# Performance work log

Measured on AMD Instinct MI355X. Metric: run time of the kernel, lower is better.

The kernel has to match this reference:

```python
import jax, jax.numpy as jnp
import numpy as np


def gcn_conv(x, src, dst, W, b, n_nodes):
    """PyG-style GCNConv: add self-loops, symmetric deg^-1/2 normalization,
    linear transform, scatter-add aggregation to dst, then bias."""
    loop = jnp.arange(n_nodes, dtype=src.dtype)
    s = jnp.concatenate([src, loop])
    d = jnp.concatenate([dst, loop])
    deg = jax.ops.segment_sum(jnp.ones_like(d, x.dtype), d, num_segments=n_nodes)
    dinv = jax.lax.rsqrt(deg)  # deg >= 1 due to self-loops
    norm = dinv[s] * dinv[d]  # [E+N]
    h = x @ W.T  # [N, out]
    msg = h[s] * norm[:, None]  # [E+N, out]
    return jax.ops.segment_sum(msg, d, num_segments=n_nodes) + b


def setup_inputs() -> dict:
    key = jax.random.key(0)
    k = jax.random.split(key, 6)
    N, E, IN, HID, OUT = 100000, 1600000, 128, 128, 64
    x = jax.random.normal(k[0], (N, IN), dtype=jnp.float32)
    edge_index = jax.random.randint(k[1], (2, E), 0, N, dtype=jnp.int64)
    W1 = jax.random.normal(k[2], (HID, IN), dtype=jnp.float32) * 0.05
    b1 = jnp.zeros((HID,), dtype=jnp.float32)
    W2 = jax.random.normal(k[3], (OUT, HID), dtype=jnp.float32) * 0.05
    b2 = jnp.zeros((OUT,), dtype=jnp.float32)
    return {"x": x, "W1": W1, "b1": b1, "W2": W2, "b2": b2, "edge_index": edge_index}


def reference(x, W1, b1, W2, b2, edge_index):
    n_nodes = x.shape[0]
    src, dst = edge_index[0], edge_index[1]
    h = jax.nn.relu(gcn_conv(x, src, dst, W1, b1, n_nodes))
    return gcn_conv(h, src, dst, W2, b2, n_nodes)
```

## Files before the change

### kernel.cpp

```cpp
#include <hip/hip_runtime.h>
#include <hip/hip_bf16.h>


#define IN_F  128
#define HID_F 128
#define OUT_F 64

#define NPB     128
#define MAXBKT  1024
#define CHUNK   2048
#define CAP     4096
#define SLAB    4096

typedef __bf16 bf16_t;
typedef __bf16 bf16x4 __attribute__((ext_vector_type(4)));
typedef __bf16 bf16x8 __attribute__((ext_vector_type(8)));
typedef float  f32x4  __attribute__((ext_vector_type(4)));

__global__ __launch_bounds__(256) void k_hist(const int* __restrict__ dst, int E,
                                              int* __restrict__ chunkhist, int NBKT,
                                              int pchunks,
                                              const float* __restrict__ W1s,
                                              const float* __restrict__ W2s,
                                              bf16_t* __restrict__ Wdst,
                                              int n1, int n2,
                                              int* __restrict__ bcur) {
    if ((int)blockIdx.x >= pchunks) {
        int i = (blockIdx.x - pchunks) * 256 + threadIdx.x;
        if (i < n1) Wdst[i] = (bf16_t)W1s[i];
        else if (i < n1 + n2) Wdst[i] = (bf16_t)W2s[i - n1];
        else if (i < n1 + n2 + NBKT) bcur[i - n1 - n2] = (i - n1 - n2) * SLAB;
        return;
    }
    __shared__ int cnt[MAXBKT];
    for (int i = threadIdx.x; i < NBKT; i += 256) cnt[i] = 0;
    __syncthreads();
    int base = blockIdx.x * CHUNK;
    for (int i = threadIdx.x; i < CHUNK; i += 256) {
        int e = base + i;
        if (e < E) atomicAdd(&cnt[dst[e] >> 7], 1);
    }
    __syncthreads();
    int* ch = chunkhist + (size_t)blockIdx.x * MAXBKT;
    for (int i = threadIdx.x; i < NBKT; i += 256) ch[i] = cnt[i];
}

__global__ __launch_bounds__(256) void k_part(const int* __restrict__ src,
                                              const int* __restrict__ dst, int E,
                                              int* __restrict__ bcur,
                                              const int* __restrict__ chunkhist,
                                              unsigned* __restrict__ part, int NBKT) {
    __shared__ int cnt[MAXBKT];
    __shared__ int base[MAXBKT];
    const int* ch = chunkhist + (size_t)blockIdx.x * MAXBKT;
    for (int i = threadIdx.x; i < NBKT; i += 256) {
        int c = ch[i];
        base[i] = c ? atomicAdd(&bcur[i], c) : 0;
        cnt[i] = 0;
    }
    __syncthreads();
    int cbase = blockIdx.x * CHUNK;
    for (int i = threadIdx.x; i < CHUNK; i += 256) {
        int e = cbase + i;
        if (e < E) {
            int d = dst[e];
            int b = d >> 7;
            int lp = atomicAdd(&cnt[b], 1);
            part[base[b] + lp] = (unsigned)src[e] | ((unsigned)(d & 127) << 17);
        }
    }
}

__global__ __launch_bounds__(256) void k_bucket(const unsigned* __restrict__ part,
                                                const int* __restrict__ bcur,
                                                int2* __restrict__ off2,
                                                int* __restrict__ col,
                                                float* __restrict__ dinv, int N) {
    __shared__ int lcnt[NPB];
    __shared__ int lexc[NPB];
    __shared__ int lcur[NPB];
    __shared__ int stage[CAP];
    int b = blockIdx.x;
    int t = threadIdx.x;
    int node0 = b * NPB;
    int nb = min(NPB, N - node0);
    int e0s = b * SLAB;
    int cnt = bcur[b] - e0s;
    if (t < NPB) lcnt[t] = 0;
    __syncthreads();
    for (int i = t; i < cnt; i += 256)
        atomicAdd(&lcnt[part[e0s + i] >> 17], 1);
    __syncthreads();
    if (t < NPB) lexc[t] = lcnt[t];
    __syncthreads();
    for (int ofs = 1; ofs < NPB; ofs <<= 1) {
        int add = (t >= ofs && t < NPB) ? lexc[t - ofs] : 0;
        __syncthreads();
        if (t < NPB) lexc[t] += add;
        __syncthreads();
    }
    if (t < NPB) {
        int ex = lexc[t] - lcnt[t];
        lcur[t] = ex;
        if (t < nb) {
            off2[node0 + t] = make_int2(e0s + ex, e0s + ex + lcnt[t]);
            dinv[node0 + t] = rsqrtf((float)lcnt[t] + 1.0f);
        }
    }
    __syncthreads();
    for (int i = t; i < cnt; i += 256) {
        unsigned p = part[e0s + i];
        int dl = p >> 17;
        int sv = (int)(p & 0x1FFFF);
        int lp = atomicAdd(&lcur[dl], 1);
        if (lp < CAP) stage[lp] = sv;
        else col[e0s + lp] = sv;
    }
    __syncthreads();
    for (int i = t; i < cnt && i < CAP; i += 256) col[e0s + i] = stage[i];
}

template <int NCOL, typename TIN>
__global__ __launch_bounds__(256) void k_gemm_mfma(const TIN* __restrict__ X,
                                                   const bf16_t* __restrict__ W,
                                                   const float* __restrict__ scale,
                                                   bf16_t* __restrict__ H, int N) {
    constexpr int CT = NCOL / 16;
    int wv = threadIdx.x >> 6, lane = threadIdx.x & 63;
    int quad = lane >> 4, l16 = lane & 15;
    int row0 = blockIdx.x * 128 + wv * 32;
    f32x4 acc[2][CT] = {};
#pragma unroll
    for (int ks = 0; ks < 4; ks++) {
        int k0 = ks * 32 + quad * 8;
        bf16x8 a[2];
#pragma unroll
        for (int rt = 0; rt < 2; rt++) {
            int r = row0 + rt * 16 + l16;
            if (r >= N) r = N - 1;
            const TIN* p = X + (size_t)r * 128 + k0;
            if constexpr (sizeof(TIN) == 4) {
                f32x4 x0 = *(const f32x4*)p;
                f32x4 x1 = *(const f32x4*)(p + 4);
                bf16x8 tt;
                tt[0] = (bf16_t)x0[0]; tt[1] = (bf16_t)x0[1];
                tt[2] = (bf16_t)x0[2]; tt[3] = (bf16_t)x0[3];
                tt[4] = (bf16_t)x1[0]; tt[5] = (bf16_t)x1[1];
                tt[6] = (bf16_t)x1[2]; tt[7] = (bf16_t)x1[3];
                a[rt] = tt;
            } else {
                a[rt] = *(const bf16x8*)p;
            }
        }
#pragma unroll
        for (int ct = 0; ct < CT; ct++) {
            bf16x8 bfrag = *(const bf16x8*)(W + (size_t)(ct * 16 + l16) * 128 + k0);
#pragma unroll
            for (int rt = 0; rt < 2; rt++)
                acc[rt][ct] = __builtin_amdgcn_mfma_f32_16x16x32_bf16(a[rt], bfrag, acc[rt][ct], 0, 0, 0);
        }
    }
#pragma unroll
    for (int rt = 0; rt < 2; rt++)
#pragma unroll
        for (int r4 = 0; r4 < 4; r4++) {
            int r = row0 + rt * 16 + quad * 4 + r4;
            if (r < N) {
                float sc = scale[r];
#pragma unroll
                for (int ct = 0; ct < CT; ct++)
                    H[(size_t)r * NCOL + ct * 16 + l16] = (bf16_t)(sc * acc[rt][ct][r4]);
            }
        }
}

template <bool RELU, typename TOUT>
__global__ __launch_bounds__(256) void k_agg128(const bf16_t* __restrict__ h,
                                                const int2* __restrict__ off2,
                                                const int* __restrict__ col,
                                                const float* __restrict__ dinv,
                                                const float* __restrict__ bias,
                                                TOUT* __restrict__ out, int N) {
    int wave = threadIdx.x >> 6;
    int lane = threadIdx.x & 63;
    int node = __builtin_amdgcn_readfirstlane(blockIdx.x * 4 + wave);
    if (node >= N) return;
    int q = lane >> 4;
    int f = (lane & 15) * 8;
    float a[8] = {0.f, 0.f, 0.f, 0.f, 0.f, 0.f, 0.f, 0.f};
    if (q == 0) {
        bf16x8 r = *(const bf16x8*)(h + (unsigned)node * 128u + f);
#pragma unroll
        for (int j = 0; j < 8; j++) a[j] = (float)r[j];
    }
    int2 oe = off2[node];
    int e0 = __builtin_amdgcn_readfirstlane(oe.x);
    int e1 = __builtin_amdgcn_readfirstlane(oe.y);
    int e = e0;
    for (; e + 8 <= e1; e += 8) {
        int4 c0 = *(const int4*)(col + e);
        int4 c1 = *(const int4*)(col + e + 4);
        int s0 = q == 0 ? c0.x : q == 1 ? c0.y : q == 2 ? c0.z : c0.w;
        int s1 = q == 0 ? c1.x : q == 1 ? c1.y : q == 2 ? c1.z : c1.w;
        bf16x8 r0 = *(const bf16x8*)(h + (unsigned)s0 * 128u + f);
        bf16x8 r1 = *(const bf16x8*)(h + (unsigned)s1 * 128u + f);
#pragma unroll
        for (int j = 0; j < 8; j++) a[j] += (float)r0[j] + (float)r1[j];
    }
    for (; e < e1; e += 4) {
        int4 c0 = *(const int4*)(col + e);
        int s0 = q == 0 ? c0.x : q == 1 ? c0.y : q == 2 ? c0.z : c0.w;
        bool act = (e + q) < e1;
        if (!act) s0 = 0;
        bf16x8 r = *(const bf16x8*)(h + (unsigned)s0 * 128u + f);
        if (act) {
#pragma unroll
            for (int j = 0; j < 8; j++) a[j] += (float)r[j];
        }
    }
#pragma unroll
    for (int j = 0; j < 8; j++) {
        a[j] += __shfl_xor(a[j], 16);
        a[j] += __shfl_xor(a[j], 32);
    }
    if (lane < 16) {
        float di = dinv[node];
        f32x4 b0 = *(const f32x4*)(bias + f);
        f32x4 b1 = *(const f32x4*)(bias + f + 4);
        float r[8];
#pragma unroll
        for (int j = 0; j < 4; j++) r[j] = a[j] * di + b0[j];
#pragma unroll
        for (int j = 0; j < 4; j++) r[4 + j] = a[4 + j] * di + b1[j];
        if (RELU) {
#pragma unroll
            for (int j = 0; j < 8; j++) r[j] = fmaxf(r[j], 0.f);
        }
        if constexpr (sizeof(TOUT) == 2) {
            bf16x8 v;
#pragma unroll
            for (int j = 0; j < 8; j++) v[j] = (bf16_t)r[j];
            *(bf16x8*)((bf16_t*)out + (unsigned)node * 128u + f) = v;
        } else {
            f32x4 v0 = {r[0], r[1], r[2], r[3]};
            f32x4 v1 = {r[4], r[5], r[6], r[7]};
            *(f32x4*)((float*)out + (unsigned)node * 128u + f) = v0;
            *(f32x4*)((float*)out + (unsigned)node * 128u + f + 4) = v1;
        }
    }
}

template <bool RELU>
__global__ __launch_bounds__(256) void k_agg64(const bf16_t* __restrict__ h,
                                               const int2* __restrict__ off2,
                                               const int* __restrict__ col,
                                               const float* __restrict__ dinv,
                                               const float* __restrict__ bias,
                                               float* __restrict__ out, int N) {
    int wave = threadIdx.x >> 6;
    int lane = threadIdx.x & 63;
    int node = __builtin_amdgcn_readfirstlane(blockIdx.x * 4 + wave);
    if (node >= N) return;
    int q = lane >> 4;
    int f = (lane & 15) * 4;
    float a0 = 0.f, a1 = 0.f, a2 = 0.f, a3 = 0.f;
    if (q == 0) {
        bf16x4 r = *(const bf16x4*)(h + (unsigned)node * 64u + f);
        a0 = (float)r[0]; a1 = (float)r[1]; a2 = (float)r[2]; a3 = (float)r[3];
    }
    int2 oe = off2[node];
    int e0 = __builtin_amdgcn_readfirstlane(oe.x);
    int e1 = __builtin_amdgcn_readfirstlane(oe.y);
    int e = e0;
    for (; e + 16 <= e1; e += 16) {
        int4 c0 = *(const int4*)(col + e);
        int4 c1 = *(const int4*)(col + e + 4);
        int4 c2 = *(const int4*)(col + e + 8);
        int4 c3 = *(const int4*)(col + e + 12);
        int s0 = q == 0 ? c0.x : q == 1 ? c0.y : q == 2 ? c0.z : c0.w;
        int s1 = q == 0 ? c1.x : q == 1 ? c1.y : q == 2 ? c1.z : c1.w;
        int s2 = q == 0 ? c2.x : q == 1 ? c2.y : q == 2 ? c2.z : c2.w;
        int s3 = q == 0 ? c3.x : q == 1 ? c3.y : q == 2 ? c3.z : c3.w;
        bf16x4 r0 = *(const bf16x4*)(h + (unsigned)s0 * 64u + f);
        bf16x4 r1 = *(const bf16x4*)(h + (unsigned)s1 * 64u + f);
        bf16x4 r2 = *(const bf16x4*)(h + (unsigned)s2 * 64u + f);
        bf16x4 r3 = *(const bf16x4*)(h + (unsigned)s3 * 64u + f);
        a0 += (float)r0[0] + (float)r1[0] + (float)r2[0] + (float)r3[0];
        a1 += (float)r0[1] + (float)r1[1] + (float)r2[1] + (float)r3[1];
        a2 += (float)r0[2] + (float)r1[2] + (float)r2[2] + (float)r3[2];
        a3 += (float)r0[3] + (float)r1[3] + (float)r2[3] + (float)r3[3];
    }
    for (; e < e1; e += 4) {
        int4 c0 = *(const int4*)(col + e);
        int s0 = q == 0 ? c0.x : q == 1 ? c0.y : q == 2 ? c0.z : c0.w;
        bool act = (e + q) < e1;
        if (!act) s0 = 0;
        bf16x4 r = *(const bf16x4*)(h + (unsigned)s0 * 64u + f);
        if (act) {
            a0 += (float)r[0]; a1 += (float)r[1];
            a2 += (float)r[2]; a3 += (float)r[3];
        }
    }
    a0 += __shfl_xor(a0, 16); a0 += __shfl_xor(a0, 32);
    a1 += __shfl_xor(a1, 16); a1 += __shfl_xor(a1, 32);
    a2 += __shfl_xor(a2, 16); a2 += __shfl_xor(a2, 32);
    a3 += __shfl_xor(a3, 16); a3 += __shfl_xor(a3, 32);
    if (lane < 16) {
        float di = dinv[node];
        f32x4 bv = *(const f32x4*)(bias + f);
        float r0 = a0 * di + bv[0];
        float r1 = a1 * di + bv[1];
        float r2 = a2 * di + bv[2];
        float r3 = a3 * di + bv[3];
        if (RELU) {
            r0 = fmaxf(r0, 0.f); r1 = fmaxf(r1, 0.f);
            r2 = fmaxf(r2, 0.f); r3 = fmaxf(r3, 0.f);
        }
        f32x4 v = {r0, r1, r2, r3};
        *(f32x4*)(out + (unsigned)node * 64u + f) = v;
    }
}

extern "C" void kernel_launch(void* const* d_in, const int* in_sizes, int n_in,
                              void* d_out, int out_size, void* d_ws, size_t ws_size,
                              hipStream_t stream) {
    const float* x  = (const float*)d_in[0];
    const float* W1 = (const float*)d_in[1];
    const float* b1 = (const float*)d_in[2];
    const float* W2 = (const float*)d_in[3];
    const float* b2 = (const float*)d_in[4];
    const int*   ei = (const int*)d_in[5];

    int N = in_sizes[0] / IN_F;
    int E = in_sizes[5] / 2;
    const int* src = ei;
    const int* dst = ei + E;
    int NBKT = (N + NPB - 1) / NPB;
    int pchunks = (E + CHUNK - 1) / CHUNK;

    size_t woff = 0;
    auto alloc = [&](size_t bytes) {
        void* p = (char*)d_ws + woff;
        woff += (bytes + 255) & ~(size_t)255;
        return p;
    };
    int*      bcur  = (int*)alloc((size_t)NBKT * 4);
    int*      chist = (int*)alloc((size_t)pchunks * MAXBKT * 4);
    unsigned* part  = (unsigned*)alloc((size_t)NBKT * SLAB * 4);
    int*      col   = (int*)alloc((size_t)NBKT * SLAB * 4);
    int2*     off2  = (int2*)alloc((size_t)N * 8);
    float*    dinv  = (float*)alloc((size_t)N * 4);
    bf16_t*   Wb    = (bf16_t*)alloc((size_t)(HID_F * IN_F + OUT_F * HID_F) * 2);
    bf16_t*   W1b   = Wb;
    bf16_t*   W2b   = Wb + HID_F * IN_F;
    bf16_t*   h1    = (bf16_t*)alloc((size_t)N * HID_F * 2);
    bf16_t*   h1r   = (bf16_t*)alloc((size_t)N * HID_F * 2);
    bf16_t*   h2    = h1;
    float*    outp  = (float*)d_out;

    int n1 = HID_F * IN_F, n2 = OUT_F * HID_F;
    int tailblocks = (n1 + n2 + NBKT + 255) / 256;
    k_hist<<<pchunks + tailblocks, 256, 0, stream>>>(dst, E, chist, NBKT, pchunks,
                                                     W1, W2, Wb, n1, n2, bcur);
    k_part<<<pchunks, 256, 0, stream>>>(src, dst, E, bcur, chist, part, NBKT);
    k_bucket<<<NBKT, 256, 0, stream>>>(part, bcur, off2, col, dinv, N);

    int gemm_blocks = (N + 127) / 128;
    int agg_blocks  = (N + 3) / 4;

    k_gemm_mfma<HID_F, float><<<gemm_blocks, 256, 0, stream>>>(x, W1b, dinv, h1, N);
    k_agg128<true, bf16_t><<<agg_blocks, 256, 0, stream>>>(h1, off2, col, dinv, b1, h1r, N);

    k_gemm_mfma<OUT_F, bf16_t><<<gemm_blocks, 256, 0, stream>>>(h1r, W2b, dinv, h2, N);
    k_agg64<false><<<agg_blocks, 256, 0, stream>>>(h2, off2, col, dinv, b2, outp, N);
}
```

Before: 304.2 us.

## Pad CSR rows to multiples of eight and map one node per sixteen lanes

The bucket kernel now pads each node's neighbor list to a multiple of 8 using a sentinel index N. The GEMM writes a zero row at index N, so the padded gathers contribute nothing and the aggregation loop has no tail handling. The aggregation kernels now give each node 16 lanes instead of a whole wave, each lane issuing 8 independent row loads per iteration, which removes the cross-quarter shuffle reduction and raises memory-level parallelism. bf16 is unpacked with manual bit shifts. The trade-offs are extra padded gathers of the cached zero row, divergence between nodes of different degree within a wave, and more slab space used by padding.

```diff
diff --git a/kernel.cpp b/kernel.cpp
--- a/kernel.cpp
+++ b/kernel.cpp
@@ -15,7 +15,10 @@
 typedef __bf16 bf16_t;
 typedef __bf16 bf16x4 __attribute__((ext_vector_type(4)));
 typedef __bf16 bf16x8 __attribute__((ext_vector_type(8)));
+typedef float  f32x2  __attribute__((ext_vector_type(2)));
 typedef float  f32x4  __attribute__((ext_vector_type(4)));
+typedef unsigned u32x2 __attribute__((ext_vector_type(2)));
+typedef unsigned u32x4 __attribute__((ext_vector_type(4)));
 
 __global__ __launch_bounds__(256) void k_hist(const int* __restrict__ dst, int E,
                                               int* __restrict__ chunkhist, int NBKT,
@@ -91,7 +94,7 @@
     for (int i = t; i < cnt; i += 256)
         atomicAdd(&lcnt[part[e0s + i] >> 17], 1);
     __syncthreads();
-    if (t < NPB) lexc[t] = lcnt[t];
+    if (t < NPB) lexc[t] = (lcnt[t] + 7) & ~7;
     __syncthreads();
     for (int ofs = 1; ofs < NPB; ofs <<= 1) {
         int add = (t >= ofs && t < NPB) ? lexc[t - ofs] : 0;
@@ -100,10 +103,11 @@
         __syncthreads();
     }
     if (t < NPB) {
-        int ex = lexc[t] - lcnt[t];
+        int pc = (lcnt[t] + 7) & ~7;
+        int ex = lexc[t] - pc;
         lcur[t] = ex;
         if (t < nb) {
-            off2[node0 + t] = make_int2(e0s + ex, e0s + ex + lcnt[t]);
+            off2[node0 + t] = make_int2(e0s + ex, e0s + ex + pc);
             dinv[node0 + t] = rsqrtf((float)lcnt[t] + 1.0f);
         }
     }
@@ -117,7 +121,15 @@
         else col[e0s + lp] = sv;
     }
     __syncthreads();
-    for (int i = t; i < cnt && i < CAP; i += 256) col[e0s + i] = stage[i];
+    if (t < NPB) {
+        int en = lexc[t];
+        for (int i = lcur[t]; i < en; i++) {
+            if (i < CAP) stage[i] = N; else col[e0s + i] = N;
+        }
+    }
+    __syncthreads();
+    int tot = lexc[NPB - 1];
+    for (int i = t; i < tot && i < CAP; i += 256) col[e0s + i] = stage[i];
 }
 
 template <int NCOL, typename TIN>
@@ -170,6 +182,10 @@
 #pragma unroll
                 for (int ct = 0; ct < CT; ct++)
                     H[(size_t)r * NCOL + ct * 16 + l16] = (bf16_t)(sc * acc[rt][ct][r4]);
+            } else if (r == N) {
+#pragma unroll
+                for (int ct = 0; ct < CT; ct++)
+                    H[(size_t)N * NCOL + ct * 16 + l16] = (bf16_t)0.f;
             }
         }
 }
@@ -181,72 +197,66 @@
                                                 const float* __restrict__ dinv,
                                                 const float* __restrict__ bias,
                                                 TOUT* __restrict__ out, int N) {
-    int wave = threadIdx.x >> 6;
     int lane = threadIdx.x & 63;
-    int node = __builtin_amdgcn_readfirstlane(blockIdx.x * 4 + wave);
+    int wv = threadIdx.x >> 6;
+    int g = lane >> 4, fl = lane & 15;
+    int node = blockIdx.x * 16 + wv * 4 + g;
     if (node >= N) return;
-    int q = lane >> 4;
-    int f = (lane & 15) * 8;
-    float a[8] = {0.f, 0.f, 0.f, 0.f, 0.f, 0.f, 0.f, 0.f};
-    if (q == 0) {
-        bf16x8 r = *(const bf16x8*)(h + (unsigned)node * 128u + f);
-#pragma unroll
-        for (int j = 0; j < 8; j++) a[j] = (float)r[j];
-    }
+    int f = fl * 8;
+    const bf16_t* hp = h + f;
+    u32x4 ws = *(const u32x4*)(hp + (unsigned)node * 128u);
     int2 oe = off2[node];
-    int e0 = __builtin_amdgcn_readfirstlane(oe.x);
-    int e1 = __builtin_amdgcn_readfirstlane(oe.y);
-    int e = e0;
-    for (; e + 8 <= e1; e += 8) {
+    f32x2 a2[4];
+#pragma unroll
+    for (int k = 0; k < 4; k++) {
+        f32x2 v;
+        v.x = __uint_as_float(ws[k] << 16);
+        v.y = __uint_as_float(ws[k] & 0xffff0000u);
+        a2[k] = v;
+    }
+    for (int e = oe.x; e < oe.y; e += 8) {
         int4 c0 = *(const int4*)(col + e);
         int4 c1 = *(const int4*)(col + e + 4);
-        int s0 = q == 0 ? c0.x : q == 1 ? c0.y : q == 2 ? c0.z : c0.w;
-        int s1 = q == 0 ? c1.x : q == 1 ? c1.y : q == 2 ? c1.z : c1.w;
-        bf16x8 r0 = *(const bf16x8*)(h + (unsigned)s0 * 128u + f);
-        bf16x8 r1 = *(const bf16x8*)(h + (unsigned)s1 * 128u + f);
-#pragma unroll
-        for (int j = 0; j < 8; j++) a[j] += (float)r0[j] + (float)r1[j];
-    }
-    for (; e < e1; e += 4) {
-        int4 c0 = *(const int4*)(col + e);
-        int s0 = q == 0 ? c0.x : q == 1 ? c0.y : q == 2 ? c0.z : c0.w;
-        bool act = (e + q) < e1;
-        if (!act) s0 = 0;
-        bf16x8 r = *(const bf16x8*)(h + (unsigned)s0 * 128u + f);
-        if (act) {
-#pragma unroll
-            for (int j = 0; j < 8; j++) a[j] += (float)r[j];
-        }
-    }
+        u32x4 w[8];
+        w[0] = *(const u32x4*)(hp + (unsigned)c0.x * 128u);
+        w[1] = *(const u32x4*)(hp + (unsigned)c0.y * 128u);
+        w[2] = *(const u32x4*)(hp + (unsigned)c0.z * 128u);
+        w[3] = *(const u32x4*)(hp + (unsigned)c0.w * 128u);
+        w[4] = *(const u32x4*)(hp + (unsigned)c1.x * 128u);
+        w[5] = *(const u32x4*)(hp + (unsigned)c1.y * 128u);
+        w[6] = *(const u32x4*)(hp + (unsigned)c1.z * 128u);
+        w[7] = *(const u32x4*)(hp + (unsigned)c1.w * 128u);
+#pragma unroll
+        for (int u = 0; u < 8; u++)
+#pragma unroll
+            for (int k = 0; k < 4; k++) {
+                f32x2 v;
+                v.x = __uint_as_float(w[u][k] << 16);
+                v.y = __uint_as_float(w[u][k] & 0xffff0000u);
+                a2[k] += v;
+            }
+    }
+    float di = dinv[node];
+    f32x4 b0 = *(const f32x4*)(bias + f);
+    f32x4 b1 = *(const f32x4*)(bias + f + 4);
+    float r[8];
 #pragma unroll
     for (int j = 0; j < 8; j++) {
-        a[j] += __shfl_xor(a[j], 16);
-        a[j] += __shfl_xor(a[j], 32);
-    }
-    if (lane < 16) {
-        float di = dinv[node];
-        f32x4 b0 = *(const f32x4*)(bias + f);
-        f32x4 b1 = *(const f32x4*)(bias + f + 4);
-        float r[8];
-#pragma unroll
-        for (int j = 0; j < 4; j++) r[j] = a[j] * di + b0[j];
-#pragma unroll
-        for (int j = 0; j < 4; j++) r[4 + j] = a[4 + j] * di + b1[j];
-        if (RELU) {
-#pragma unroll
-            for (int j = 0; j < 8; j++) r[j] = fmaxf(r[j], 0.f);
-        }
-        if constexpr (sizeof(TOUT) == 2) {
-            bf16x8 v;
-#pragma unroll
-            for (int j = 0; j < 8; j++) v[j] = (bf16_t)r[j];
-            *(bf16x8*)((bf16_t*)out + (unsigned)node * 128u + f) = v;
-        } else {
-            f32x4 v0 = {r[0], r[1], r[2], r[3]};
-            f32x4 v1 = {r[4], r[5], r[6], r[7]};
-            *(f32x4*)((float*)out + (unsigned)node * 128u + f) = v0;
-            *(f32x4*)((float*)out + (unsigned)node * 128u + f + 4) = v1;
-        }
+        float bv = (j < 4) ? b0[j] : b1[j - 4];
+        float val = a2[j >> 1][j & 1] * di + bv;
+        if (RELU) val = fmaxf(val, 0.f);
+        r[j] = val;
+    }
+    if constexpr (sizeof(TOUT) == 2) {
+        bf16x8 v;
+#pragma unroll
+        for (int j = 0; j < 8; j++) v[j] = (bf16_t)r[j];
+        *(bf16x8*)((bf16_t*)out + (unsigned)node * 128u + f) = v;
+    } else {
+        f32x4 v0 = {r[0], r[1], r[2], r[3]};
+        f32x4 v1 = {r[4], r[5], r[6], r[7]};
+        *(f32x4*)((float*)out + (unsigned)node * 128u + f) = v0;
+        *(f32x4*)((float*)out + (unsigned)node * 128u + f + 4) = v1;
     }
 }
 
@@ -257,68 +267,57 @@
                                                const float* __restrict__ dinv,
                                                const float* __restrict__ bias,
                                                float* __restrict__ out, int N) {
-    int wave = threadIdx.x >> 6;
     int lane = threadIdx.x & 63;
-    int node = __builtin_amdgcn_readfirstlane(blockIdx.x * 4 + wave);
+    int wv = threadIdx.x >> 6;
+    int g = lane >> 4, fl = lane & 15;
+    int node = blockIdx.x * 16 + wv * 4 + g;
     if (node >= N) return;
-    int q = lane >> 4;
-    int f = (lane & 15) * 4;
-    float a0 = 0.f, a1 = 0.f, a2 = 0.f, a3 = 0.f;
-    if (q == 0) {
-        bf16x4 r = *(const bf16x4*)(h + (unsigned)node * 64u + f);
-        a0 = (float)r[0]; a1 = (float)r[1]; a2 = (float)r[2]; a3 = (float)r[3];
-    }
+    int f = fl * 4;
+    const bf16_t* hp = h + f;
+    u32x2 ws = *(const u32x2*)(hp + (unsigned)node * 64u);
     int2 oe = off2[node];
-    int e0 = __builtin_amdgcn_readfirstlane(oe.x);
-    int e1 = __builtin_amdgcn_readfirstlane(oe.y);
-    int e = e0;
-    for (; e + 16 <= e1; e += 16) {
+    f32x2 a2[2];
+#pragma unroll
+    for (int k = 0; k < 2; k++) {
+        f32x2 v;
+        v.x = __uint_as_float(ws[k] << 16);
+        v.y = __uint_as_float(ws[k] & 0xffff0000u);
+        a2[k] = v;
+    }
+    for (int e = oe.x; e < oe.y; e += 8) {
         int4 c0 = *(const int4*)(col + e);
         int4 c1 = *(const int4*)(col + e + 4);
-        int4 c2 = *(const int4*)(col + e + 8);
-        int4 c3 = *(const int4*)(col + e + 12);
-        int s0 = q == 0 ? c0.x : q == 1 ? c0.y : q == 2 ? c0.z : c0.w;
-        int s1 = q == 0 ? c1.x : q == 1 ? c1.y : q == 2 ? c1.z : c1.w;
-        int s2 = q == 0 ? c2.x : q == 1 ? c2.y : q == 2 ? c2.z : c2.w;
-        int s3 = q == 0 ? c3.x : q == 1 ? c3.y : q == 2 ? c3.z : c3.w;
-        bf16x4 r0 = *(const bf16x4*)(h + (unsigned)s0 * 64u + f);
-        bf16x4 r1 = *(const bf16x4*)(h + (unsigned)s1 * 64u + f);
-        bf16x4 r2 = *(const bf16x4*)(h + (unsigned)s2 * 64u + f);
-        bf16x4 r3 = *(const bf16x4*)(h + (unsigned)s3 * 64u + f);
-        a0 += (float)r0[0] + (float)r1[0] + (float)r2[0] + (float)r3[0];
-        a1 += (float)r0[1] + (float)r1[1] + (float)r2[1] + (float)r3[1];
-        a2 += (float)r0[2] + (float)r1[2] + (float)r2[2] + (float)r3[2];
-        a3 += (float)r0[3] + (float)r1[3] + (float)r2[3] + (float)r3[3];
-    }
-    for (; e < e1; e += 4) {
-        int4 c0 = *(const int4*)(col + e);
-        int s0 = q == 0 ? c0.x : q == 1 ? c0.y : q == 2 ? c0.z : c0.w;
-        bool act = (e + q) < e1;
-        if (!act) s0 = 0;
-        bf16x4 r = *(const bf16x4*)(h + (unsigned)s0 * 64u + f);
-        if (act) {
-            a0 += (float)r[0]; a1 += (float)r[1];
-            a2 += (float)r[2]; a3 += (float)r[3];
-        }
-    }
-    a0 += __shfl_xor(a0, 16); a0 += __shfl_xor(a0, 32);
-    a1 += __shfl_xor(a1, 16); a1 += __shfl_xor(a1, 32);
-    a2 += __shfl_xor(a2, 16); a2 += __shfl_xor(a2, 32);
-    a3 += __shfl_xor(a3, 16); a3 += __shfl_xor(a3, 32);
-    if (lane < 16) {
-        float di = dinv[node];
-        f32x4 bv = *(const f32x4*)(bias + f);
-        float r0 = a0 * di + bv[0];
-        float r1 = a1 * di + bv[1];
-        float r2 = a2 * di + bv[2];
-        float r3 = a3 * di + bv[3];
-        if (RELU) {
-            r0 = fmaxf(r0, 0.f); r1 = fmaxf(r1, 0.f);
-            r2 = fmaxf(r2, 0.f); r3 = fmaxf(r3, 0.f);
-        }
-        f32x4 v = {r0, r1, r2, r3};
-        *(f32x4*)(out + (unsigned)node * 64u + f) = v;
-    }
+        u32x2 w[8];
+        w[0] = *(const u32x2*)(hp + (unsigned)c0.x * 64u);
+        w[1] = *(const u32x2*)(hp + (unsigned)c0.y * 64u);
+        w[2] = *(const u32x2*)(hp + (unsigned)c0.z * 64u);
+        w[3] = *(const u32x2*)(hp + (unsigned)c0.w * 64u);
+        w[4] = *(const u32x2*)(hp + (unsigned)c1.x * 64u);
+        w[5] = *(const u32x2*)(hp + (unsigned)c1.y * 64u);
+        w[6] = *(const u32x2*)(hp + (unsigned)c1.z * 64u);
+        w[7] = *(const u32x2*)(hp + (unsigned)c1.w * 64u);
+#pragma unroll
+        for (int u = 0; u < 8; u++)
+#pragma unroll
+            for (int k = 0; k < 2; k++) {
+                f32x2 v;
+                v.x = __uint_as_float(w[u][k] << 16);
+                v.y = __uint_as_float(w[u][k] & 0xffff0000u);
+                a2[k] += v;
+            }
+    }
+    float di = dinv[node];
+    f32x4 bv = *(const f32x4*)(bias + f);
+    float r0 = a2[0].x * di + bv[0];
+    float r1 = a2[0].y * di + bv[1];
+    float r2 = a2[1].x * di + bv[2];
+    float r3 = a2[1].y * di + bv[3];
+    if (RELU) {
+        r0 = fmaxf(r0, 0.f); r1 = fmaxf(r1, 0.f);
+        r2 = fmaxf(r2, 0.f); r3 = fmaxf(r3, 0.f);
+    }
+    f32x4 v = {r0, r1, r2, r3};
+    *(f32x4*)(out + (unsigned)node * 64u + f) = v;
 }
 
 extern "C" void kernel_launch(void* const* d_in, const int* in_sizes, int n_in,
@@ -353,7 +352,7 @@
     bf16_t*   Wb    = (bf16_t*)alloc((size_t)(HID_F * IN_F + OUT_F * HID_F) * 2);
     bf16_t*   W1b   = Wb;
     bf16_t*   W2b   = Wb + HID_F * IN_F;
-    bf16_t*   h1    = (bf16_t*)alloc((size_t)N * HID_F * 2);
+    bf16_t*   h1    = (bf16_t*)alloc((size_t)(N + 1) * HID_F * 2);
     bf16_t*   h1r   = (bf16_t*)alloc((size_t)N * HID_F * 2);
     bf16_t*   h2    = h1;
     float*    outp  = (float*)d_out;
@@ -366,7 +365,7 @@
     k_bucket<<<NBKT, 256, 0, stream>>>(part, bcur, off2, col, dinv, N);
 
     int gemm_blocks = (N + 127) / 128;
-    int agg_blocks  = (N + 3) / 4;
+    int agg_blocks  = (N + 15) / 16;
 
     k_gemm_mfma<HID_F, float><<<gemm_blocks, 256, 0, stream>>>(x, W1b, dinv, h1, N);
     k_agg128<true, bf16_t><<<agg_blocks, 256, 0, stream>>>(h1, off2, col, dinv, b1, h1r, N);
```

Result: faster. 284.2 us (-6.6%).
